# Optimization experiments

Hardware: AMD Instinct MI355X
Metric: run time of the kernel (lower is better)

The kernel has to match this reference:

```python
import jax, jax.numpy as jnp
import numpy as np

B, D, H, L = 65536, 512, 1024, 64
LOG2PI = float(np.log(2.0 * np.pi))


def setup_inputs() -> dict:
    key = jax.random.key(0)
    ks = jax.random.split(key, 16)
    s = jnp.float32(0.02)

    def w(k, shape):
        return jax.random.normal(k, shape, dtype=jnp.float32) * s

    return {
        "x": jax.random.normal(ks[0], (B, D), dtype=jnp.float32),
        "eps": jax.random.normal(ks[1], (B, L), dtype=jnp.float32),
        # encoder params (Linear stored as [in, out] for x @ W + b)
        "W_enc_h": w(ks[2], (D, H)), "b_enc_h": jnp.zeros((H,), jnp.float32),
        "W_enc_mu": w(ks[3], (H, L)), "b_enc_mu": jnp.zeros((L,), jnp.float32),
        "W_enc_lv": w(ks[4], (H, L)), "b_enc_lv": jnp.zeros((L,), jnp.float32),
        # decoder params
        "W_dec_h": w(ks[5], (L, H)), "b_dec_h": jnp.zeros((H,), jnp.float32),
        "W_dec_mu": w(ks[6], (H, D)), "b_dec_mu": jnp.zeros((D,), jnp.float32),
        "W_dec_lv": w(ks[7], (H, D)), "b_dec_lv": jnp.zeros((D,), jnp.float32),
    }


def reference(x, eps, W_enc_h, b_enc_h, W_enc_mu, b_enc_mu, W_enc_lv, b_enc_lv,
              W_dec_h, b_dec_h, W_dec_mu, b_dec_mu, W_dec_lv, b_dec_lv):
    beta = jnp.float32(1.0)
    # encoder
    h = jnp.tanh(x @ W_enc_h + b_enc_h)                      # [B, H]
    mu_z = h @ W_enc_mu + b_enc_mu                           # [B, L]
    lv_z = h @ W_enc_lv + b_enc_lv                           # [B, L]
    # reparameterised sample
    z = mu_z + jnp.exp(0.5 * lv_z) * eps                     # [B, L]
    # decoder
    hd = jnp.tanh(z @ W_dec_h + b_dec_h)                     # [B, H]
    mu_x = jax.nn.softmax(hd @ W_dec_mu + b_dec_mu, axis=-1) # [B, D]
    lv_x = hd @ W_dec_lv + b_dec_lv                          # [B, D]
    # KL(q(z|x) || N(0, I))
    kl = -0.5 * jnp.sum(1.0 + lv_z - mu_z ** 2 - jnp.exp(lv_z), axis=-1)  # [B]
    # diagonal Gaussian log-likelihood (closed form of MultivariateNormal
    # with diag_embed(exp(ln_var)) covariance)
    ln_pxz = -0.5 * jnp.sum(lv_x + (x - mu_x) ** 2 * jnp.exp(-lv_x) + LOG2PI, axis=-1)  # [B]
    return jnp.mean(ln_pxz - beta * kl)
```

## Files before the change

### kernel.cpp

```cpp
#include <hip/hip_runtime.h>

typedef unsigned char u8;
typedef unsigned short u16;
typedef unsigned int u32;
typedef long i64;
typedef __attribute__((ext_vector_type(2))) long long2v;
typedef __attribute__((ext_vector_type(4))) float floatx4;

#define LOG2PI_F 1.8378770664093453f

__device__ __forceinline__ u16 f2bf(float f) {
  union { float f; u32 i; } c; c.f = f;
  u32 i = c.i;
  u32 r = (i + 0x7fffu + ((i >> 16) & 1u)) >> 16;
  return (u16)r;
}
__device__ __forceinline__ float bf2f(u16 u) {
  union { u32 i; float f; } c; c.i = ((u32)u) << 16; return c.f;
}
__device__ __forceinline__ u8 f2fp8(float f) {
  int p = __builtin_amdgcn_cvt_pk_fp8_f32(f, f, 0, false);
  return (u8)(p & 0xff);
}
__device__ __forceinline__ u32 pk4fp8(float a, float b, float c, float d) {
  int lo = __builtin_amdgcn_cvt_pk_fp8_f32(a, b, 0, false);
  int v  = __builtin_amdgcn_cvt_pk_fp8_f32(c, d, lo, true);
  return (u32)v;
}
__device__ __forceinline__ void llds16(const void* g, void* l) {
  __builtin_amdgcn_global_load_lds(
      (const __attribute__((address_space(1))) u32*)g,
      (__attribute__((address_space(3))) u32*)l, 16, 0, 0);
}
__device__ __forceinline__ u32 permk(u32 k) {
  u32 g = k & ~63u, o = (k >> 3) & 7u, r = k & 7u;
  u32 po = ((o & 3u) << 1) | (o >> 2);
  return g | (po << 3) | r;
}

#define INV_4096  2.44140625e-4f
#define INV_16384 6.103515625e-5f

__global__ void pack_xb(const float* __restrict__ in, u32* __restrict__ out, int n4) {
  int i = blockIdx.x * 256 + threadIdx.x;
  if (i >= n4) return;
  const float4 v = ((const float4*)in)[i];
  int row = i >> 7;
  int k = (i & 127) << 2;
  int kp = permk(k);
  out[(row << 7) + (kp >> 2)] = pk4fp8(v.x * 16.f, v.y * 16.f, v.z * 16.f, v.w * 16.f);
}

__global__ void pack_wt(const float* __restrict__ W, u8* __restrict__ Wt, int K, int N) {
  int idx = blockIdx.x * 256 + threadIdx.x;
  if (idx >= K * N) return;
  int k = idx / N, n = idx - k * N;
  Wt[(size_t)n * K + permk(k)] = f2fp8(W[idx] * 256.f);
}

__global__ void pack_wt2(const float* __restrict__ W1, const float* __restrict__ W2,
                         u8* __restrict__ Wt, int K, int N1, int N2) {
  int idx = blockIdx.x * 256 + threadIdx.x;
  if (idx >= (N1 + N2) * K) return;
  int n = idx / K, k = idx - n * K;
  float v = (n < N1) ? W1[(size_t)k * N1 + n] : W2[(size_t)k * N2 + (n - N1)];
  Wt[(size_t)n * K + permk(k)] = f2fp8(v * 256.f);
}

__global__ void catf(const float* __restrict__ a, const float* __restrict__ b,
                     float* __restrict__ o, int n1, int n2) {
  int i = blockIdx.x * 256 + threadIdx.x;
  if (i < n1) o[i] = a[i];
  else if (i < n1 + n2) o[i] = b[i - n1];
}

template <int EPI>
__global__ __launch_bounds__(256) void gemm_bt(
    const u8* __restrict__ A, const u8* __restrict__ Bt,
    const float* __restrict__ bias, void* __restrict__ Cv,
    float inv, float outs, int M, int N, int K) {
  __shared__ __align__(16) u8 As[128 * 64];
  __shared__ __align__(16) u8 Bs[128 * 64];
  const int t = threadIdx.x;
  const int wave = t >> 6, lane = t & 63;
  const int quad = lane >> 4, l16 = lane & 15;
  const int bm = blockIdx.y * 128, bn = blockIdx.x * 128;
  const int wm = (wave >> 1) * 64, wn = (wave & 1) * 64;

  floatx4 acc[4][4];
#pragma unroll
  for (int i = 0; i < 4; ++i)
#pragma unroll
    for (int j = 0; j < 4; ++j) acc[i][j] = (floatx4){0.f, 0.f, 0.f, 0.f};

  for (int kt = 0; kt < K; kt += 64) {
#pragma unroll
    for (int i = 0; i < 2; ++i) {
      int c = i * 256 + t;
      int r = c >> 2, kcS = c & 3;
      int kc = kcS ^ ((r >> 1) & 3);
      llds16(A + (size_t)(bm + r) * K + kt + kc * 16, &As[c * 16]);
      llds16(Bt + (size_t)(bn + r) * K + kt + kc * 16, &Bs[c * 16]);
    }
    __builtin_amdgcn_s_waitcnt(0);
    __syncthreads();

    long2v a2[4], b2[4];
#pragma unroll
    for (int mi = 0; mi < 4; ++mi) {
      int m = wm + mi * 16 + l16;
      a2[mi] = *(const long2v*)&As[(4 * m + (quad ^ ((m >> 1) & 3))) * 16];
    }
#pragma unroll
    for (int ni = 0; ni < 4; ++ni) {
      int n = wn + ni * 16 + l16;
      b2[ni] = *(const long2v*)&Bs[(4 * n + (quad ^ ((n >> 1) & 3))) * 16];
    }
#pragma unroll
    for (int h = 0; h < 2; ++h)
#pragma unroll
      for (int mi = 0; mi < 4; ++mi)
#pragma unroll
        for (int ni = 0; ni < 4; ++ni)
          acc[mi][ni] = __builtin_amdgcn_mfma_f32_16x16x32_fp8_fp8(
              a2[mi][h], b2[ni][h], acc[mi][ni], 0, 0, 0);
    __syncthreads();
  }

#pragma unroll
  for (int ni = 0; ni < 4; ++ni) {
    int col = bn + wn + ni * 16 + l16;
    float bv = bias[col];
#pragma unroll
    for (int mi = 0; mi < 4; ++mi) {
#pragma unroll
      for (int r = 0; r < 4; ++r) {
        int row = bm + wm + mi * 16 + quad * 4 + r;
        float v = acc[mi][ni][r] * inv + bv;
        if (EPI == 0) {
          ((u8*)Cv)[(size_t)row * N + permk(col)] = f2fp8(tanhf(v) * outs);
        } else {
          ((u16*)Cv)[(size_t)row * N + col] = f2bf(v);
        }
      }
    }
  }
}

template <int EPI>
__global__ __launch_bounds__(512, 2) void gemm256(
    const u8* __restrict__ A, const u8* __restrict__ Bt,
    const float* __restrict__ bias, void* __restrict__ Cv,
    float inv, float outs, int M, int N, int K) {
  __shared__ __align__(16) u8 lds[4][2][256 * 64];
  const int t = threadIdx.x;
  const int wave = t >> 6, lane = t & 63;
  const int quad = lane >> 4, l16 = lane & 15;
  const int nbx = N >> 8;
  const int nwg = nbx * (M >> 8);
  int raw = blockIdx.x + nbx * blockIdx.y;
  int wgid = ((nwg & 7) == 0) ? ((raw & 7) * (nwg >> 3) + (raw >> 3)) : raw;
  const int bm = (wgid / nbx) << 8, bn = (wgid % nbx) << 8;
  const int wm = (wave >> 2) * 128, wn = (wave & 3) * 64;
  const int nt = K >> 6;

  auto stage = [&](int b, int kt) {
#pragma unroll
    for (int i = 0; i < 2; ++i) {
      int c = i * 512 + t;
      int r = c >> 2, kcS = c & 3;
      int kc = kcS ^ ((r >> 1) & 3);
      llds16(A + (size_t)(bm + r) * K + kt + kc * 16, &lds[b][0][c * 16]);
    }
#pragma unroll
    for (int i = 0; i < 2; ++i) {
      int c = i * 512 + t;
      int r = c >> 2, kcS = c & 3;
      int kc = kcS ^ ((r >> 1) & 3);
      llds16(Bt + (size_t)(bn + r) * K + kt + kc * 16, &lds[b][1][c * 16]);
    }
  };

  floatx4 acc[8][4];
#pragma unroll
  for (int i = 0; i < 8; ++i)
#pragma unroll
    for (int j = 0; j < 4; ++j) acc[i][j] = (floatx4){0.f, 0.f, 0.f, 0.f};

  stage(0, 0);
  if (nt > 1) stage(1, 64);
  if (nt > 2) stage(2, 128);

  for (int ti = 0; ti < nt; ++ti) {
    const int b = ti & 3;
    if (ti + 3 < nt) stage((ti + 3) & 3, (ti + 3) << 6);
    int rem = nt - 1 - ti;
    if (rem >= 3)      { asm volatile("s_waitcnt vmcnt(12)" ::: "memory"); }
    else if (rem == 2) { asm volatile("s_waitcnt vmcnt(8)" ::: "memory"); }
    else if (rem == 1) { asm volatile("s_waitcnt vmcnt(4)" ::: "memory"); }
    else               { asm volatile("s_waitcnt vmcnt(0)" ::: "memory"); }
    __builtin_amdgcn_s_barrier();

    const u8* As = &lds[b][0][0];
    const u8* Bs = &lds[b][1][0];
    long2v a2[8], b2[4];
#pragma unroll
    for (int mi = 0; mi < 8; ++mi) {
      int m = wm + mi * 16 + l16;
      a2[mi] = *(const long2v*)&As[(4 * m + (quad ^ ((m >> 1) & 3))) * 16];
    }
#pragma unroll
    for (int ni = 0; ni < 4; ++ni) {
      int n = wn + ni * 16 + l16;
      b2[ni] = *(const long2v*)&Bs[(4 * n + (quad ^ ((n >> 1) & 3))) * 16];
    }
    __builtin_amdgcn_s_setprio(1);
#pragma unroll
    for (int h = 0; h < 2; ++h)
#pragma unroll
      for (int mi = 0; mi < 8; ++mi)
#pragma unroll
        for (int ni = 0; ni < 4; ++ni)
          acc[mi][ni] = __builtin_amdgcn_mfma_f32_16x16x32_fp8_fp8(
              a2[mi][h], b2[ni][h], acc[mi][ni], 0, 0, 0);
    __builtin_amdgcn_s_setprio(0);
    asm volatile("s_waitcnt lgkmcnt(0)" ::: "memory");
    __builtin_amdgcn_sched_barrier(0);
    __builtin_amdgcn_s_barrier();
  }

#pragma unroll
  for (int ni = 0; ni < 4; ++ni) {
    int col = bn + wn + ni * 16 + l16;
    float bv = bias[col];
#pragma unroll
    for (int mi = 0; mi < 8; ++mi) {
#pragma unroll
      for (int r = 0; r < 4; ++r) {
        int row = bm + wm + mi * 16 + quad * 4 + r;
        float v = acc[mi][ni][r] * inv + bv;
        if (EPI == 0) {
          ((u8*)Cv)[(size_t)row * N + permk(col)] = f2fp8(tanhf(v) * outs);
        } else {
          ((u16*)Cv)[(size_t)row * N + col] = f2bf(v);
        }
      }
    }
  }
}

__global__ __launch_bounds__(256) void gemm_z(
    const u8* __restrict__ A, const u8* __restrict__ Bt,
    const float* __restrict__ bias, const float* __restrict__ eps,
    u8* __restrict__ z, float* __restrict__ accp, int M, int K) {
  __shared__ __align__(16) u8 As[128 * 64];
  __shared__ __align__(16) u8 Bs[128 * 64];
  __shared__ float sexp[128 * 64];
  const int t = threadIdx.x;
  const int wave = t >> 6, lane = t & 63;
  const int quad = lane >> 4, l16 = lane & 15;
  const int bm = blockIdx.y * 128;
  const int wm = (wave >> 1) * 64, wn = (wave & 1) * 64;

  floatx4 acc[4][4];
#pragma unroll
  for (int i = 0; i < 4; ++i)
#pragma unroll
    for (int j = 0; j < 4; ++j) acc[i][j] = (floatx4){0.f, 0.f, 0.f, 0.f};

  for (int kt = 0; kt < K; kt += 64) {
#pragma unroll
    for (int i = 0; i < 2; ++i) {
      int c = i * 256 + t;
      int r = c >> 2, kcS = c & 3;
      int kc = kcS ^ ((r >> 1) & 3);
      llds16(A + (size_t)(bm + r) * K + kt + kc * 16, &As[c * 16]);
      llds16(Bt + (size_t)r * K + kt + kc * 16, &Bs[c * 16]);
    }
    __builtin_amdgcn_s_waitcnt(0);
    __syncthreads();

    long2v a2[4], b2[4];
#pragma unroll
    for (int mi = 0; mi < 4; ++mi) {
      int m = wm + mi * 16 + l16;
      a2[mi] = *(const long2v*)&As[(4 * m + (quad ^ ((m >> 1) & 3))) * 16];
    }
#pragma unroll
    for (int ni = 0; ni < 4; ++ni) {
      int n = wn + ni * 16 + l16;
      b2[ni] = *(const long2v*)&Bs[(4 * n + (quad ^ ((n >> 1) & 3))) * 16];
    }
#pragma unroll
    for (int h = 0; h < 2; ++h)
#pragma unroll
      for (int mi = 0; mi < 4; ++mi)
#pragma unroll
        for (int ni = 0; ni < 4; ++ni)
          acc[mi][ni] = __builtin_amdgcn_mfma_f32_16x16x32_fp8_fp8(
              a2[mi][h], b2[ni][h], acc[mi][ni], 0, 0, 0);
    __syncthreads();
  }

  const bool is_lv = (wave & 1);
  float kl = 0.f;
#pragma unroll
  for (int ni = 0; ni < 4; ++ni) {
    int col = wn + ni * 16 + l16;
    float bv = bias[col];
#pragma unroll
    for (int mi = 0; mi < 4; ++mi) {
#pragma unroll
      for (int r = 0; r < 4; ++r) {
        int row = wm + mi * 16 + quad * 4 + r;
        float v = acc[mi][ni][r] * INV_16384 + bv;
        if (is_lv) {
          kl += 1.0f + v - __expf(v);
          sexp[row * 64 + (col - 64)] = __expf(0.5f * v);
        } else {
          kl -= v * v;
        }
      }
    }
  }
  __syncthreads();
  if (!is_lv) {
#pragma unroll
    for (int ni = 0; ni < 4; ++ni) {
      int col = wn + ni * 16 + l16;
      float bv = bias[col];
#pragma unroll
      for (int mi = 0; mi < 4; ++mi) {
#pragma unroll
        for (int r = 0; r < 4; ++r) {
          int row = wm + mi * 16 + quad * 4 + r;
          float mu = acc[mi][ni][r] * INV_16384 + bv;
          size_t grow = (size_t)(bm + row);
          float ep = eps[grow * 64 + col];
          z[grow * 64 + permk(col)] = f2fp8((mu + sexp[row * 64 + col] * ep) * 16.f);
        }
      }
    }
  }
  kl *= 0.5f;
  for (int off = 32; off > 0; off >>= 1) kl += __shfl_xor(kl, off, 64);
  __shared__ float s4[4];
  if (lane == 0) s4[wave] = kl;
  __syncthreads();
  if (t == 0) atomicAdd(accp, s4[0] + s4[1] + s4[2] + s4[3]);
}

__global__ __launch_bounds__(256) void lik_kernel(
    const u16* __restrict__ loglv, const float* __restrict__ x,
    float* __restrict__ acc) {
  typedef __attribute__((ext_vector_type(8))) short short8;
  const int wave = threadIdx.x >> 6, lane = threadIdx.x & 63;
  float wacc = 0.f;
  for (int rr = 0; rr < 8; ++rr) {
    int row = blockIdx.x * 32 + wave * 8 + rr;
    const u16* Lr = loglv + (size_t)row * 1024;
    short8 lg8 = ((const short8*)Lr)[lane];
    float lg[8];
#pragma unroll
    for (int j = 0; j < 8; ++j) lg[j] = bf2f((u16)lg8[j]);
    float mx = lg[0];
#pragma unroll
    for (int j = 1; j < 8; ++j) mx = fmaxf(mx, lg[j]);
    for (int off = 32; off > 0; off >>= 1) mx = fmaxf(mx, __shfl_xor(mx, off, 64));
    float e[8], s = 0.f;
#pragma unroll
    for (int j = 0; j < 8; ++j) { e[j] = __expf(lg[j] - mx); s += e[j]; }
    for (int off = 32; off > 0; off >>= 1) s += __shfl_xor(s, off, 64);
    float inv_s = 1.0f / s;
    short8 lv8 = ((const short8*)Lr)[64 + lane];
    const float* xr = x + (size_t)row * 512 + lane * 8;
    float4 x0 = *(const float4*)xr, x1 = *(const float4*)(xr + 4);
    float xs[8] = {x0.x, x0.y, x0.z, x0.w, x1.x, x1.y, x1.z, x1.w};
    float T = 0.f;
#pragma unroll
    for (int j = 0; j < 8; ++j) {
      float lv = bf2f((u16)lv8[j]);
      float d = xs[j] - e[j] * inv_s;
      T += lv + d * d * __expf(-lv) + LOG2PI_F;
    }
    for (int off = 32; off > 0; off >>= 1) T += __shfl_xor(T, off, 64);
    if (lane == 0) wacc += -0.5f * T;
  }
  __shared__ float s4[4];
  if (lane == 0) s4[wave] = wacc;
  __syncthreads();
  if (threadIdx.x == 0) atomicAdd(acc, s4[0] + s4[1] + s4[2] + s4[3]);
}

__global__ void fin_kernel(const float* __restrict__ acc, float* __restrict__ out) {
  out[0] = acc[0] * (1.0f / 65536.0f);
}

extern "C" void kernel_launch(void* const* d_in, const int* in_sizes, int n_in,
                              void* d_out, int out_size, void* d_ws, size_t ws_size,
                              hipStream_t stream) {
  const int B = 65536, D = 512, H = 1024, L = 64;
  const float* x       = (const float*)d_in[0];
  const float* eps     = (const float*)d_in[1];
  const float* W_enc_h = (const float*)d_in[2];
  const float* b_enc_h = (const float*)d_in[3];
  const float* W_enc_mu= (const float*)d_in[4];
  const float* b_enc_mu= (const float*)d_in[5];
  const float* W_enc_lv= (const float*)d_in[6];
  const float* b_enc_lv= (const float*)d_in[7];
  const float* W_dec_h = (const float*)d_in[8];
  const float* b_dec_h = (const float*)d_in[9];
  const float* W_dec_mu= (const float*)d_in[10];
  const float* b_dec_mu= (const float*)d_in[11];
  const float* W_dec_lv= (const float*)d_in[12];
  const float* b_dec_lv= (const float*)d_in[13];

  char* ws = (char*)d_ws;
  u8*   Wt_eh  = (u8*)(ws + 0);
  u8*   Wt_z   = (u8*)(ws + 524288);
  u8*   Wt_dh  = (u8*)(ws + 655360);
  u8*   Wt_dx  = (u8*)(ws + 720896);
  float* bh    = (float*)(ws + 2097152);
  float* bz    = (float*)(ws + 2101248);
  float* bdh   = (float*)(ws + 2105344);
  float* bdx   = (float*)(ws + 2109440);
  float* acc   = (float*)(ws + 2113536);
  u8*   hbuf   = (u8*)(ws + 4194304);
  u8*   xb     = (u8*)(ws + 71303168);
  u8*   zbuf   = (u8*)(ws + 104857600);
  u16*  loglv  = (u16*)(ws + 109051904);

  hipMemsetAsync(acc, 0, 256, stream);

  pack_xb<<<(B * D / 4 + 255) / 256, 256, 0, stream>>>(x, (u32*)xb, B * D / 4);
  pack_wt<<<(D * H + 255) / 256, 256, 0, stream>>>(W_enc_h, Wt_eh, D, H);
  pack_wt2<<<(H * 2 * L + 255) / 256, 256, 0, stream>>>(W_enc_mu, W_enc_lv, Wt_z, H, L, L);
  pack_wt<<<(L * H + 255) / 256, 256, 0, stream>>>(W_dec_h, Wt_dh, L, H);
  pack_wt2<<<(H * 2 * D + 255) / 256, 256, 0, stream>>>(W_dec_mu, W_dec_lv, Wt_dx, H, D, D);
  catf<<<(H + 255) / 256, 256, 0, stream>>>(b_enc_h, b_enc_h, bh, H, 0);
  catf<<<(2 * L + 255) / 256, 256, 0, stream>>>(b_enc_mu, b_enc_lv, bz, L, L);
  catf<<<(H + 255) / 256, 256, 0, stream>>>(b_dec_h, b_dec_h, bdh, H, 0);
  catf<<<(2 * D + 255) / 256, 256, 0, stream>>>(b_dec_mu, b_dec_lv, bdx, D, D);

  gemm256<0><<<dim3(H / 256, B / 256), 512, 0, stream>>>(
      xb, Wt_eh, bh, hbuf, INV_4096, 64.f, B, H, D);
  gemm_z<<<dim3(1, B / 128), 256, 0, stream>>>(hbuf, Wt_z, bz, eps, zbuf, acc, B, H);
  gemm_bt<0><<<dim3(H / 128, B / 128), 256, 0, stream>>>(
      zbuf, Wt_dh, bdh, hbuf, INV_4096, 64.f, B, H, L);
  gemm256<2><<<dim3(1024 / 256, B / 256), 512, 0, stream>>>(
      hbuf, Wt_dx, bdx, loglv, INV_16384, 0.f, B, 1024, H);
  lik_kernel<<<B / 32, 256, 0, stream>>>(loglv, x, acc);
  fin_kernel<<<1, 1, 0, stream>>>(acc, (float*)d_out);
}
```

Baseline: 640.4 us.

## Stage GEMM epilogues through LDS and interleave fragment loads with MFMAs

Result: faster. 594.5 us (-7.2%).

```diff
diff --git a/kernel.cpp b/kernel.cpp
--- a/kernel.cpp
+++ b/kernel.cpp
@@ -74,13 +74,13 @@
   else if (i < n1 + n2) o[i] = b[i - n1];
 }
 
-template <int EPI>
-__global__ __launch_bounds__(256) void gemm_bt(
+__global__ __launch_bounds__(256) void gemm_bt0(
     const u8* __restrict__ A, const u8* __restrict__ Bt,
-    const float* __restrict__ bias, void* __restrict__ Cv,
+    const float* __restrict__ bias, u8* __restrict__ C,
     float inv, float outs, int M, int N, int K) {
-  __shared__ __align__(16) u8 As[128 * 64];
-  __shared__ __align__(16) u8 Bs[128 * 64];
+  __shared__ __align__(16) u8 smem[16384];
+  u8* As = smem;
+  u8* Bs = smem + 8192;
   const int t = threadIdx.x;
   const int wave = t >> 6, lane = t & 63;
   const int quad = lane >> 4, l16 = lane & 15;
@@ -129,21 +129,26 @@
 
 #pragma unroll
   for (int ni = 0; ni < 4; ++ni) {
-    int col = bn + wn + ni * 16 + l16;
-    float bv = bias[col];
+    int col = wn + ni * 16 + l16;
+    float bv = bias[bn + col];
+    u32 pc = permk((u32)col);
 #pragma unroll
     for (int mi = 0; mi < 4; ++mi) {
 #pragma unroll
       for (int r = 0; r < 4; ++r) {
-        int row = bm + wm + mi * 16 + quad * 4 + r;
+        int row = wm + mi * 16 + quad * 4 + r;
         float v = acc[mi][ni][r] * inv + bv;
-        if (EPI == 0) {
-          ((u8*)Cv)[(size_t)row * N + permk(col)] = f2fp8(tanhf(v) * outs);
-        } else {
-          ((u16*)Cv)[(size_t)row * N + col] = f2bf(v);
-        }
+        smem[row * 128 + pc] = f2fp8(tanhf(v) * outs);
       }
     }
+  }
+  __syncthreads();
+#pragma unroll
+  for (int j = 0; j < 4; ++j) {
+    int u = j * 256 + t;
+    int row = u >> 3, c16 = u & 7;
+    *(long2v*)(C + (size_t)(bm + row) * N + bn + c16 * 16) =
+        *(const long2v*)&smem[row * 128 + c16 * 16];
   }
 }
 
@@ -164,7 +169,9 @@
   const int wm = (wave >> 2) * 128, wn = (wave & 3) * 64;
   const int nt = K >> 6;
 
-  auto stage = [&](int b, int kt) {
+  auto stage = [&](int ti) {
+    const int b = ti & 3;
+    const int kt = ti << 6;
 #pragma unroll
     for (int i = 0; i < 2; ++i) {
       int c = i * 512 + t;
@@ -181,70 +188,135 @@
     }
   };
 
+  int offA[8], offB[4];
+#pragma unroll
+  for (int mi = 0; mi < 8; ++mi) {
+    int m = wm + mi * 16 + l16;
+    offA[mi] = (4 * m + (quad ^ ((m >> 1) & 3))) * 16;
+  }
+#pragma unroll
+  for (int ni = 0; ni < 4; ++ni) {
+    int n = wn + ni * 16 + l16;
+    offB[ni] = (4 * n + (quad ^ ((n >> 1) & 3))) * 16;
+  }
+
   floatx4 acc[8][4];
 #pragma unroll
   for (int i = 0; i < 8; ++i)
 #pragma unroll
     for (int j = 0; j < 4; ++j) acc[i][j] = (floatx4){0.f, 0.f, 0.f, 0.f};
 
-  stage(0, 0);
-  if (nt > 1) stage(1, 64);
-  if (nt > 2) stage(2, 128);
-
-  for (int ti = 0; ti < nt; ++ti) {
-    const int b = ti & 3;
-    if (ti + 3 < nt) stage((ti + 3) & 3, (ti + 3) << 6);
-    int rem = nt - 1 - ti;
-    if (rem >= 3)      { asm volatile("s_waitcnt vmcnt(12)" ::: "memory"); }
-    else if (rem == 2) { asm volatile("s_waitcnt vmcnt(8)" ::: "memory"); }
-    else if (rem == 1) { asm volatile("s_waitcnt vmcnt(4)" ::: "memory"); }
-    else               { asm volatile("s_waitcnt vmcnt(0)" ::: "memory"); }
-    __builtin_amdgcn_s_barrier();
-
-    const u8* As = &lds[b][0][0];
-    const u8* Bs = &lds[b][1][0];
-    long2v a2[8], b2[4];
-#pragma unroll
-    for (int mi = 0; mi < 8; ++mi) {
-      int m = wm + mi * 16 + l16;
-      a2[mi] = *(const long2v*)&As[(4 * m + (quad ^ ((m >> 1) & 3))) * 16];
-    }
+  long2v a2[8], b2[4], b3[4];
+
+  stage(0);
+  stage(1);
+  asm volatile("s_waitcnt vmcnt(4)" ::: "memory");
+  __builtin_amdgcn_s_barrier();
+  asm volatile("" ::: "memory");
+  {
+    const u8* bA = &lds[0][0][0];
+    const u8* bB = &lds[0][1][0];
+#pragma unroll
+    for (int ni = 0; ni < 4; ++ni) b2[ni] = *(const long2v*)(bB + offB[ni]);
+#pragma unroll
+    for (int mi = 0; mi < 8; ++mi) a2[mi] = *(const long2v*)(bA + offA[mi]);
+  }
+
+#define GBODY(TI, BCUR, BNXT) {                                               \
+    const int ti_ = (TI);                                                     \
+    if (ti_ + 2 < nt) {                                                       \
+      stage(ti_ + 2);                                                         \
+      asm volatile("s_waitcnt vmcnt(4)" ::: "memory");                        \
+    } else {                                                                  \
+      asm volatile("s_waitcnt vmcnt(0)" ::: "memory");                        \
+    }                                                                         \
+    __builtin_amdgcn_s_barrier();                                             \
+    asm volatile("" ::: "memory");                                            \
+    const u8* bA_ = &lds[(ti_ + 1) & 3][0][0];                                \
+    const u8* bB_ = &lds[(ti_ + 1) & 3][1][0];                                \
+    _Pragma("unroll")                                                         \
+    for (int ni = 0; ni < 4; ++ni) BNXT[ni] = *(const long2v*)(bB_ + offB[ni]);\
+    __builtin_amdgcn_s_setprio(1);                                            \
+    _Pragma("unroll")                                                         \
+    for (int mi = 0; mi < 8; ++mi) {                                          \
+      _Pragma("unroll")                                                       \
+      for (int h = 0; h < 2; ++h)                                             \
+        _Pragma("unroll")                                                     \
+        for (int ni = 0; ni < 4; ++ni)                                        \
+          acc[mi][ni] = __builtin_amdgcn_mfma_f32_16x16x32_fp8_fp8(           \
+              a2[mi][h], BCUR[ni][h], acc[mi][ni], 0, 0, 0);                  \
+      a2[mi] = *(const long2v*)(bA_ + offA[mi]);                              \
+    }                                                                         \
+    __builtin_amdgcn_s_setprio(0);                                            \
+  }
+
+  int ti = 0;
+  for (; ti + 2 < nt; ti += 2) {
+    GBODY(ti, b2, b3);
+    GBODY(ti + 1, b3, b2);
+  }
+  GBODY(ti, b2, b3);
+#undef GBODY
+  __builtin_amdgcn_s_setprio(1);
+#pragma unroll
+  for (int mi = 0; mi < 8; ++mi)
+#pragma unroll
+    for (int h = 0; h < 2; ++h)
+#pragma unroll
+      for (int ni = 0; ni < 4; ++ni)
+        acc[mi][ni] = __builtin_amdgcn_mfma_f32_16x16x32_fp8_fp8(
+            a2[mi][h], b3[ni][h], acc[mi][ni], 0, 0, 0);
+  __builtin_amdgcn_s_setprio(0);
+
+  __syncthreads();
+  u8* eb = &lds[0][0][0];
+  if (EPI == 0) {
 #pragma unroll
     for (int ni = 0; ni < 4; ++ni) {
-      int n = wn + ni * 16 + l16;
-      b2[ni] = *(const long2v*)&Bs[(4 * n + (quad ^ ((n >> 1) & 3))) * 16];
-    }
-    __builtin_amdgcn_s_setprio(1);
-#pragma unroll
-    for (int h = 0; h < 2; ++h)
-#pragma unroll
-      for (int mi = 0; mi < 8; ++mi)
-#pragma unroll
-        for (int ni = 0; ni < 4; ++ni)
-          acc[mi][ni] = __builtin_amdgcn_mfma_f32_16x16x32_fp8_fp8(
-              a2[mi][h], b2[ni][h], acc[mi][ni], 0, 0, 0);
-    __builtin_amdgcn_s_setprio(0);
-    asm volatile("s_waitcnt lgkmcnt(0)" ::: "memory");
-    __builtin_amdgcn_sched_barrier(0);
-    __builtin_amdgcn_s_barrier();
-  }
-
-#pragma unroll
-  for (int ni = 0; ni < 4; ++ni) {
-    int col = bn + wn + ni * 16 + l16;
-    float bv = bias[col];
-#pragma unroll
-    for (int mi = 0; mi < 8; ++mi) {
-#pragma unroll
-      for (int r = 0; r < 4; ++r) {
-        int row = bm + wm + mi * 16 + quad * 4 + r;
-        float v = acc[mi][ni][r] * inv + bv;
-        if (EPI == 0) {
-          ((u8*)Cv)[(size_t)row * N + permk(col)] = f2fp8(tanhf(v) * outs);
-        } else {
-          ((u16*)Cv)[(size_t)row * N + col] = f2bf(v);
+      int col = wn + ni * 16 + l16;
+      float bv = bias[bn + col];
+      u32 pc = permk((u32)col);
+#pragma unroll
+      for (int mi = 0; mi < 8; ++mi) {
+#pragma unroll
+        for (int r = 0; r < 4; ++r) {
+          int row = wm + mi * 16 + quad * 4 + r;
+          float v = acc[mi][ni][r] * inv + bv;
+          eb[row * 256 + pc] = f2fp8(tanhf(v) * outs);
         }
       }
+    }
+    __syncthreads();
+#pragma unroll
+    for (int j = 0; j < 8; ++j) {
+      int u = j * 512 + t;
+      int row = u >> 4, c16 = u & 15;
+      *(long2v*)((u8*)Cv + (size_t)(bm + row) * N + bn + c16 * 16) =
+          *(const long2v*)&eb[row * 256 + c16 * 16];
+    }
+  } else {
+    u16* ebw = (u16*)eb;
+#pragma unroll
+    for (int ni = 0; ni < 4; ++ni) {
+      int col = wn + ni * 16 + l16;
+      float bv = bias[bn + col];
+#pragma unroll
+      for (int mi = 0; mi < 8; ++mi) {
+#pragma unroll
+        for (int r = 0; r < 4; ++r) {
+          int row = wm + mi * 16 + quad * 4 + r;
+          float v = acc[mi][ni][r] * inv + bv;
+          ebw[row * 256 + col] = f2bf(v);
+        }
+      }
+    }
+    __syncthreads();
+#pragma unroll
+    for (int j = 0; j < 16; ++j) {
+      int u = j * 512 + t;
+      int row = u >> 5, c16 = u & 31;
+      *(long2v*)((u16*)Cv + (size_t)(bm + row) * N + bn + c16 * 8) =
+          *(const long2v*)&ebw[row * 256 + c16 * 8];
     }
   }
 }
@@ -445,7 +517,7 @@
   gemm256<0><<<dim3(H / 256, B / 256), 512, 0, stream>>>(
       xb, Wt_eh, bh, hbuf, INV_4096, 64.f, B, H, D);
   gemm_z<<<dim3(1, B / 128), 256, 0, stream>>>(hbuf, Wt_z, bz, eps, zbuf, acc, B, H);
-  gemm_bt<0><<<dim3(H / 128, B / 128), 256, 0, stream>>>(
+  gemm_bt0<<<dim3(H / 128, B / 128), 256, 0, stream>>>(
       zbuf, Wt_dh, bdh, hbuf, INV_4096, 64.f, B, H, L);
   gemm256<2><<<dim3(1024 / 256, B / 256), 512, 0, stream>>>(
       hbuf, Wt_dx, bdx, loglv, INV_16384, 0.f, B, 1024, H);
```
